# Performance work log

Hardware: AMD Instinct MI355X
Metric: run time of the kernel (lower is better)

## Reference

```python
import jax, jax.numpy as jnp
import numpy as np

N = 100000
E = 1000000
IN_FEAT = 64
OUT_FEAT = 64


def setup_inputs() -> dict:
    key = jax.random.key(0)
    k_h, k_src, k_dst, k_w, k_b = jax.random.split(key, 5)
    h = jax.random.normal(k_h, (N, IN_FEAT), dtype=jnp.float32)
    src = jax.random.randint(k_src, (E,), 0, N, dtype=jnp.int64)
    dst = jax.random.randint(k_dst, (E,), 0, N, dtype=jnp.int64)
    # nn.Linear(in_feat*2, out_feat): W is [out, 2*in], b is [out]
    bound = 1.0 / np.sqrt(2 * IN_FEAT)
    W = jax.random.uniform(k_w, (OUT_FEAT, 2 * IN_FEAT), dtype=jnp.float32, minval=-bound, maxval=bound)
    b = jax.random.uniform(k_b, (OUT_FEAT,), dtype=jnp.float32, minval=-bound, maxval=bound)
    return {"h": h, "src": src, "dst": dst, "W": W, "b": b}


def reference(h, src, dst, W, b):
    # copy_u + mean: gather src features, segment-mean over dst (in-neighbors)
    msg_sum = jax.ops.segment_sum(h[src], dst, num_segments=N)          # [N, in]
    deg = jax.ops.segment_sum(jnp.ones((src.shape[0],), h.dtype), dst, num_segments=N)  # [N]
    h_neigh = msg_sum / jnp.maximum(deg, 1.0)[:, None]                  # isolated nodes -> 0 (DGL mean)
    h_total = jnp.concatenate([h, h_neigh], axis=1)                     # [N, 2*in]
    return jax.nn.relu(h_total @ W.T + b)
```

## Files before the change

### kernel.cpp

```cpp
#include <hip/hip_runtime.h>

#define FEAT 64
#define BN 128
#define SHIFTMAXB 512
#define BCAP 4096

typedef __attribute__((ext_vector_type(8))) __bf16 bf16x8;
typedef __attribute__((ext_vector_type(8))) unsigned short ushort8;
typedef __attribute__((ext_vector_type(4))) float f32x4;

__device__ inline unsigned short f2bf(float f) {
    union { float f; unsigned u; } c; c.f = f;
    unsigned u = c.u;
    return (unsigned short)((u + 0x7fffu + ((u >> 16) & 1u)) >> 16);
}
__device__ inline float bf2f(unsigned short s) {
    union { unsigned u; float f; } c; c.u = ((unsigned)s) << 16; return c.f;
}

__global__ void __launch_bounds__(256)
zero_kernel(int* __restrict__ p)
{
    int t = threadIdx.x;
    p[t] = 0; p[t + 256] = 0;
}

__global__ void __launch_bounds__(256)
scatter_kernel(const float* __restrict__ h, unsigned short* __restrict__ hbf,
               int total8, const float* __restrict__ W,
               unsigned short* __restrict__ wfg,
               const int* __restrict__ src, const int* __restrict__ dst,
               int* __restrict__ cursors, int* __restrict__ pairs,
               int E, int shift, int h2bfB)
{
    __shared__ int hist[512];
    __shared__ int chunk[512];
    int bid = blockIdx.x, t = threadIdx.x;

    if (bid < h2bfB) {
        int i = bid * 256 + t;
        if (i < total8) {
            const float4* p = (const float4*)(h + (size_t)i * 8);
            float4 a = p[0], b = p[1];
            ushort8 v;
            v[0] = f2bf(a.x); v[1] = f2bf(a.y); v[2] = f2bf(a.z); v[3] = f2bf(a.w);
            v[4] = f2bf(b.x); v[5] = f2bf(b.y); v[6] = f2bf(b.z); v[7] = f2bf(b.w);
            *(ushort8*)(hbf + (size_t)i * 8) = v;
        }
        return;
    }
    if (bid < h2bfB + 4) {
        int i = (bid - h2bfB) * 256 + t;
        int ksnt = i >> 6, lane = i & 63;
        int row = (ksnt & 3) * 16 + (lane & 15);
        int kb  = (ksnt >> 2) * 32 + (lane >> 4) * 8;
        const float4* p = (const float4*)(W + row * 128 + kb);
        float4 a = p[0], b = p[1];
        ushort8 v;
        v[0] = f2bf(a.x); v[1] = f2bf(a.y); v[2] = f2bf(a.z); v[3] = f2bf(a.w);
        v[4] = f2bf(b.x); v[5] = f2bf(b.y); v[6] = f2bf(b.z); v[7] = f2bf(b.w);
        *(ushort8*)(wfg + i * 8) = v;
        return;
    }

    hist[t] = 0; hist[t + 256] = 0;
    __syncthreads();
    int base = (bid - h2bfB - 4) * 4096;
    int s_[16], d_[16];
    #pragma unroll
    for (int r = 0; r < 4; ++r) {
        int e = base + r * 1024 + t * 4;
        if (e + 3 < E) {
            *(int4*)&s_[r * 4] = *(const int4*)&src[e];
            *(int4*)&d_[r * 4] = *(const int4*)&dst[e];
        } else {
            #pragma unroll
            for (int j = 0; j < 4; ++j) {
                int ee = e + j;
                s_[r * 4 + j] = (ee < E) ? src[ee] : -1;
                d_[r * 4 + j] = (ee < E) ? dst[ee] : -1;
            }
        }
    }
    #pragma unroll
    for (int i = 0; i < 16; ++i)
        if (d_[i] >= 0) atomicAdd(&hist[d_[i] >> shift], 1);
    __syncthreads();
    if (hist[t])       { chunk[t]       = (t)       * BCAP + atomicAdd(&cursors[t],       hist[t]);       hist[t] = 0; }
    if (hist[t + 256]) { chunk[t + 256] = (t + 256) * BCAP + atomicAdd(&cursors[t + 256], hist[t + 256]); hist[t + 256] = 0; }
    __syncthreads();
    int mask = (1 << shift) - 1;
    #pragma unroll
    for (int i = 0; i < 16; ++i) {
        if (d_[i] >= 0) {
            int bk = d_[i] >> shift;
            int pos = atomicAdd(&hist[bk], 1);
            int at  = chunk[bk] + pos;
            if (at < (bk + 1) * BCAP)
                pairs[at] = (s_[i] << shift) | (d_[i] & mask);
        }
    }
}

__device__ inline void scan_bases(const int* __restrict__ sizes,
                                  int* __restrict__ basesl, int* __restrict__ sums)
{
    int t = threadIdx.x;
    int v0 = sizes[2 * t], v1 = sizes[2 * t + 1];
    int s = v0 + v1;
    sums[t] = s; __syncthreads();
    for (int o = 1; o < 256; o <<= 1) {
        int u = (t >= o) ? sums[t - o] : 0;
        __syncthreads();
        sums[t] += u; __syncthreads();
    }
    int ex = sums[t] - s;
    basesl[2 * t] = ex; basesl[2 * t + 1] = ex + v0;
    __syncthreads();
}

__global__ void __launch_bounds__(256)
bucket_csr_kernel(const int* __restrict__ pairs, const int* __restrict__ cursors,
                  int* __restrict__ off, int* __restrict__ adj,
                  int N, int E, int shift)
{
    __shared__ int basesl[512];
    __shared__ int sums[256];
    __shared__ int cnt[256];
    int b = blockIdx.x, t = threadIdx.x;

    scan_bases(cursors, basesl, sums);

    int nb0 = b << shift;
    int nn = min(1 << shift, N - nb0);
    int mask = (1 << shift) - 1;
    int e0 = basesl[b];
    int sz = cursors[b];
    int p0 = b * BCAP;

    cnt[t] = 0; __syncthreads();
    for (int e = t; e < sz; e += 256)
        atomicAdd(&cnt[pairs[p0 + e] & mask], 1);
    __syncthreads();
    int v = cnt[t];
    sums[t] = v; __syncthreads();
    for (int o = 1; o < 256; o <<= 1) {
        int u = (t >= o) ? sums[t - o] : 0;
        __syncthreads();
        sums[t] += u; __syncthreads();
    }
    int ex = sums[t] - v;
    if (t < nn) off[nb0 + t] = e0 + ex;
    cnt[t] = ex;
    __syncthreads();
    for (int e = t; e < sz; e += 256) {
        int pk = pairs[p0 + e];
        int pos = atomicAdd(&cnt[pk & mask], 1);
        adj[e0 + pos] = pk >> shift;
    }
    if (b == 0 && t == 0) off[N] = E;
}

__global__ void __launch_bounds__(256)
gather_kernel(const unsigned short* __restrict__ hbf, const int* __restrict__ adj,
              const int* __restrict__ off, unsigned short* __restrict__ hn,
              int N)
{
    int node = (blockIdx.x * 256 + threadIdx.x) >> 6;
    if (node >= N) return;
    int lane = threadIdx.x & 63;
    int sub = lane >> 3, f8 = lane & 7;

    int o0 = off[node], o1 = off[node + 1];
    int deg = o1 - o0;
    int adjv = (o0 + lane < o1) ? adj[o0 + lane] : 0;

    float acc[8] = {0.f, 0.f, 0.f, 0.f, 0.f, 0.f, 0.f, 0.f};
    int nb = (min(deg, 64) + 7) >> 3;
    for (int k = 0; k < nb; k += 2) {
        int eA = k * 8 + sub, eB = (k + 1) * 8 + sub;
        int iA = __shfl(adjv, eA);
        int iB = __shfl(adjv, eB);
        bool vA = eA < deg;
        bool vB = (k + 1 < nb) && (eB < deg);
        ushort8 rA, rB;
        if (vA) rA = *(const ushort8*)&hbf[(size_t)iA * FEAT + f8 * 8];
        if (vB) rB = *(const ushort8*)&hbf[(size_t)iB * FEAT + f8 * 8];
        if (vA) {
            #pragma unroll
            for (int j = 0; j < 8; ++j) acc[j] += bf2f(rA[j]);
        }
        if (vB) {
            #pragma unroll
            for (int j = 0; j < 8; ++j) acc[j] += bf2f(rB[j]);
        }
    }
    for (int base = o0 + 64; base < o1; base += 8) {
        int e = base + sub;
        if (e < o1) {
            ushort8 r = *(const ushort8*)&hbf[(size_t)adj[e] * FEAT + f8 * 8];
            #pragma unroll
            for (int j = 0; j < 8; ++j) acc[j] += bf2f(r[j]);
        }
    }
    #pragma unroll
    for (int j = 0; j < 8; ++j) {
        float v = acc[j];
        v += __shfl_xor(v, 8);
        v += __shfl_xor(v, 16);
        v += __shfl_xor(v, 32);
        acc[j] = v;
    }
    if (sub == 0) {
        float inv = 1.0f / fmaxf((float)deg, 1.0f);
        ushort8 m;
        #pragma unroll
        for (int j = 0; j < 8; ++j) m[j] = f2bf(acc[j] * inv);
        *(ushort8*)&hn[(size_t)node * 128 + f8 * 8] = m;
    }
}

__global__ void __launch_bounds__(512, 3)
sage_mfma_kernel(const unsigned short* __restrict__ hbf,
                 const unsigned short* __restrict__ hn,
                 const unsigned short* __restrict__ wfg,
                 const float* __restrict__ bias, float* __restrict__ out, int N)
{
    __shared__ unsigned short xl[BN * 128];
    __shared__ unsigned short wl[1024 * 8];

    int t = threadIdx.x;
    int lane = t & 63, w = t >> 6;
    int node0 = blockIdx.x * BN;

    #pragma unroll
    for (int it = 0; it < 2; ++it) {
        int i = t + it * 512;
        *(ushort8*)&wl[i * 8] = *(const ushort8*)&wfg[(size_t)i * 8];
    }

    #pragma unroll
    for (int it = 0; it < 2; ++it) {
        int i = t + it * 512;
        int n = i >> 3, c8 = i & 7;
        int node = node0 + n;
        ushort8 v = {};
        if (node < N) v = *(const ushort8*)&hbf[(size_t)node * FEAT + c8 * 8];
        *(ushort8*)&xl[(n * 16 + (c8 ^ (n & 7))) * 8] = v;
    }

    #pragma unroll
    for (int it = 0; it < 2; ++it) {
        int i = t + it * 512;
        int n = i >> 3, c8 = i & 7;
        int node = node0 + n;
        ushort8 v = {};
        if (node < N) v = *(const ushort8*)&hn[(size_t)node * 128 + c8 * 8];
        *(ushort8*)&xl[(n * 16 + ((8 + c8) ^ (n & 7))) * 8] = v;
    }
    __syncthreads();

    f32x4 acc[4] = {};
    int r = w * 16 + (lane & 15);
    #pragma unroll
    for (int ks = 0; ks < 4; ++ks) {
        int chunk = ks * 4 + (lane >> 4);
        bf16x8 a = *(const bf16x8*)&xl[(r * 16 + (chunk ^ (r & 7))) * 8];
        #pragma unroll
        for (int nt = 0; nt < 4; ++nt) {
            bf16x8 b = *(const bf16x8*)&wl[((ks * 4 + nt) * 64 + lane) * 8];
            acc[nt] = __builtin_amdgcn_mfma_f32_16x16x32_bf16(a, b, acc[nt], 0, 0, 0);
        }
    }

    int col   = lane & 15;
    int rbase = node0 + w * 16 + (lane >> 4) * 4;
    #pragma unroll
    for (int nt = 0; nt < 4; ++nt) {
        float bj = bias[nt * 16 + col];
        #pragma unroll
        for (int rr = 0; rr < 4; ++rr) {
            int node = rbase + rr;
            if (node < N) {
                float vv = acc[nt][rr] + bj;
                out[(size_t)node * FEAT + nt * 16 + col] = fmaxf(vv, 0.f);
            }
        }
    }
}

extern "C" void kernel_launch(void* const* d_in, const int* in_sizes, int n_in,
                              void* d_out, int out_size, void* d_ws, size_t ws_size,
                              hipStream_t stream)
{
    const float* h   = (const float*)d_in[0];
    const int*   src = (const int*)d_in[1];
    const int*   dst = (const int*)d_in[2];
    const float* W   = (const float*)d_in[3];
    const float* b   = (const float*)d_in[4];
    float* out = (float*)d_out;

    int N = in_sizes[0] / FEAT;
    int E = in_sizes[1];

    int shift = 0;
    while (((N - 1) >> shift) >= SHIFTMAXB) ++shift;
    int NB = ((N - 1) >> shift) + 1;

    unsigned short* hbf = (unsigned short*)d_ws;
    unsigned short* wfg = hbf + (size_t)N * FEAT;
    int*  pairs   = (int*)(wfg + 8192);
    int*  adj     = pairs + (size_t)512 * BCAP;
    int*  off     = adj + E;
    int*  cursors = off + (N + 1);

    zero_kernel<<<1, 256, 0, stream>>>(cursors);

    int total8 = N * (FEAT / 8);
    int h2bfB  = (total8 + 255) / 256;
    int spB    = (E + 4095) / 4096;
    scatter_kernel<<<h2bfB + 4 + spB, 256, 0, stream>>>(h, hbf, total8, W, wfg,
                                                        src, dst, cursors, pairs,
                                                        E, shift, h2bfB);

    bucket_csr_kernel<<<NB, 256, 0, stream>>>(pairs, cursors, off, adj, N, E, shift);

    unsigned short* hn = (unsigned short*)d_out;
    int gwaves = (N + 3) / 4;
    gather_kernel<<<gwaves, 256, 0, stream>>>(hbf, adj, off, hn, N);

    int gblocks = (N + BN - 1) / BN;
    sage_mfma_kernel<<<gblocks, 512, 0, stream>>>(hbf, hn, wfg, b, out, N);
}
```

Before: 89.26 us.

## Fuse neighbor gather into MFMA linear kernel via shared memory

Merges the separate gather and MFMA GEMM kernels into one kernel. Each 1024-thread block aggregates 16 nodes, one wave per node, writes the bf16 means and self features into LDS, then four waves run the 16x64 MFMA with bias and ReLU. This removes the global round trip of the intermediate neighbor buffer and one kernel launch. In exchange, every block reloads the full weight tile into LDS, and only 4 of 16 waves do the GEMM after a block-wide barrier, which may reduce gather occupancy.

```diff
diff --git a/kernel.cpp b/kernel.cpp
--- a/kernel.cpp
+++ b/kernel.cpp
@@ -1,7 +1,6 @@
 #include <hip/hip_runtime.h>
 
 #define FEAT 64
-#define BN 128
 #define SHIFTMAXB 512
 #define BCAP 4096
 
@@ -161,17 +160,31 @@
     if (b == 0 && t == 0) off[N] = E;
 }
 
-__global__ void __launch_bounds__(256)
-gather_kernel(const unsigned short* __restrict__ hbf, const int* __restrict__ adj,
-              const int* __restrict__ off, unsigned short* __restrict__ hn,
-              int N)
-{
-    int node = (blockIdx.x * 256 + threadIdx.x) >> 6;
-    if (node >= N) return;
-    int lane = threadIdx.x & 63;
+__global__ void __launch_bounds__(1024, 8)
+gather_mfma_kernel(const unsigned short* __restrict__ hbf,
+                   const int* __restrict__ adj, const int* __restrict__ off,
+                   const unsigned short* __restrict__ wfg,
+                   const float* __restrict__ bias, float* __restrict__ out, int N)
+{
+    __shared__ unsigned short xl[16 * 128];
+    __shared__ unsigned short wl[1024 * 8];
+
+    int t = threadIdx.x;
+    int lane = t & 63, w = t >> 6;
+    int node0 = blockIdx.x * 16;
+    int node = node0 + w;
+    bool valid = node < N;
     int sub = lane >> 3, f8 = lane & 7;
 
-    int o0 = off[node], o1 = off[node + 1];
+    *(ushort8*)&wl[t * 8] = *(const ushort8*)&wfg[(size_t)t * 8];
+
+    if (valid && sub == 1) {
+        ushort8 v = *(const ushort8*)&hbf[(size_t)node * FEAT + f8 * 8];
+        *(ushort8*)&xl[(w * 16 + (f8 ^ (w & 7))) * 8] = v;
+    }
+
+    int o0 = 0, o1 = 0;
+    if (valid) { o0 = off[node]; o1 = off[node + 1]; }
     int deg = o1 - o0;
     int adjv = (o0 + lane < o1) ? adj[o0 + lane] : 0;
 
@@ -211,80 +224,32 @@
         v += __shfl_xor(v, 32);
         acc[j] = v;
     }
-    if (sub == 0) {
+    if (valid && sub == 0) {
         float inv = 1.0f / fmaxf((float)deg, 1.0f);
         ushort8 m;
         #pragma unroll
         for (int j = 0; j < 8; ++j) m[j] = f2bf(acc[j] * inv);
-        *(ushort8*)&hn[(size_t)node * 128 + f8 * 8] = m;
-    }
-}
-
-__global__ void __launch_bounds__(512, 3)
-sage_mfma_kernel(const unsigned short* __restrict__ hbf,
-                 const unsigned short* __restrict__ hn,
-                 const unsigned short* __restrict__ wfg,
-                 const float* __restrict__ bias, float* __restrict__ out, int N)
-{
-    __shared__ unsigned short xl[BN * 128];
-    __shared__ unsigned short wl[1024 * 8];
-
-    int t = threadIdx.x;
-    int lane = t & 63, w = t >> 6;
-    int node0 = blockIdx.x * BN;
-
-    #pragma unroll
-    for (int it = 0; it < 2; ++it) {
-        int i = t + it * 512;
-        *(ushort8*)&wl[i * 8] = *(const ushort8*)&wfg[(size_t)i * 8];
-    }
-
-    #pragma unroll
-    for (int it = 0; it < 2; ++it) {
-        int i = t + it * 512;
-        int n = i >> 3, c8 = i & 7;
-        int node = node0 + n;
-        ushort8 v = {};
-        if (node < N) v = *(const ushort8*)&hbf[(size_t)node * FEAT + c8 * 8];
-        *(ushort8*)&xl[(n * 16 + (c8 ^ (n & 7))) * 8] = v;
-    }
-
-    #pragma unroll
-    for (int it = 0; it < 2; ++it) {
-        int i = t + it * 512;
-        int n = i >> 3, c8 = i & 7;
-        int node = node0 + n;
-        ushort8 v = {};
-        if (node < N) v = *(const ushort8*)&hn[(size_t)node * 128 + c8 * 8];
-        *(ushort8*)&xl[(n * 16 + ((8 + c8) ^ (n & 7))) * 8] = v;
-    }
-    __syncthreads();
-
-    f32x4 acc[4] = {};
-    int r = w * 16 + (lane & 15);
-    #pragma unroll
-    for (int ks = 0; ks < 4; ++ks) {
-        int chunk = ks * 4 + (lane >> 4);
-        bf16x8 a = *(const bf16x8*)&xl[(r * 16 + (chunk ^ (r & 7))) * 8];
+        *(ushort8*)&xl[(w * 16 + ((8 + f8) ^ (w & 7))) * 8] = m;
+    }
+    __syncthreads();
+
+    if (w < 4) {
+        f32x4 gacc = {};
+        int r = lane & 15;
         #pragma unroll
-        for (int nt = 0; nt < 4; ++nt) {
-            bf16x8 b = *(const bf16x8*)&wl[((ks * 4 + nt) * 64 + lane) * 8];
-            acc[nt] = __builtin_amdgcn_mfma_f32_16x16x32_bf16(a, b, acc[nt], 0, 0, 0);
-        }
-    }
-
-    int col   = lane & 15;
-    int rbase = node0 + w * 16 + (lane >> 4) * 4;
-    #pragma unroll
-    for (int nt = 0; nt < 4; ++nt) {
-        float bj = bias[nt * 16 + col];
+        for (int ks = 0; ks < 4; ++ks) {
+            int chunk = ks * 4 + (lane >> 4);
+            bf16x8 a = *(const bf16x8*)&xl[(r * 16 + (chunk ^ (r & 7))) * 8];
+            bf16x8 b = *(const bf16x8*)&wl[((ks * 4 + w) * 64 + lane) * 8];
+            gacc = __builtin_amdgcn_mfma_f32_16x16x32_bf16(a, b, gacc, 0, 0, 0);
+        }
+        int col = lane & 15;
+        float bj = bias[w * 16 + col];
         #pragma unroll
         for (int rr = 0; rr < 4; ++rr) {
-            int node = rbase + rr;
-            if (node < N) {
-                float vv = acc[nt][rr] + bj;
-                out[(size_t)node * FEAT + nt * 16 + col] = fmaxf(vv, 0.f);
-            }
+            int nd = node0 + (lane >> 4) * 4 + rr;
+            if (nd < N)
+                out[(size_t)nd * FEAT + w * 16 + col] = fmaxf(gacc[rr] + bj, 0.f);
         }
     }
 }
@@ -325,10 +290,6 @@
 
     bucket_csr_kernel<<<NB, 256, 0, stream>>>(pairs, cursors, off, adj, N, E, shift);
 
-    unsigned short* hn = (unsigned short*)d_out;
-    int gwaves = (N + 3) / 4;
-    gather_kernel<<<gwaves, 256, 0, stream>>>(hbf, adj, off, hn, N);
-
-    int gblocks = (N + BN - 1) / BN;
-    sage_mfma_kernel<<<gblocks, 512, 0, stream>>>(hbf, hn, wfg, b, out, N);
-}
+    int gblocks = (N + 15) / 16;
+    gather_mfma_kernel<<<gblocks, 1024, 0, stream>>>(hbf, adj, off, wfg, b, out, N);
+}
```

Measured after the change: 98.79 us. +10.7%, slower.

## Fuse bucket CSR build and neighbor gather into one LDS-resident kernel

Applied to the files above, without the earlier changes.

Merges the per-bucket CSR construction and the mean-aggregation gather into one kernel. Each 1024-thread block sorts its bucket's edges into a local adjacency list in shared memory, then 16 waves each aggregate 16 nodes from it. This removes the global adj/off arrays, their writes and re-reads, the cross-bucket base scan, and one kernel launch. The cost is far fewer blocks (one per bucket), with each wave walking its nodes one after another, which may hurt latency hiding and load balance across CUs.

```diff
diff --git a/kernel.cpp b/kernel.cpp
--- a/kernel.cpp
+++ b/kernel.cpp
@@ -102,121 +102,89 @@
     }
 }
 
-__device__ inline void scan_bases(const int* __restrict__ sizes,
-                                  int* __restrict__ basesl, int* __restrict__ sums)
-{
-    int t = threadIdx.x;
-    int v0 = sizes[2 * t], v1 = sizes[2 * t + 1];
-    int s = v0 + v1;
-    sums[t] = s; __syncthreads();
+__global__ void __launch_bounds__(1024, 2)
+bucket_gather_kernel(const unsigned short* __restrict__ hbf,
+                     const int* __restrict__ pairs, const int* __restrict__ cursors,
+                     unsigned short* __restrict__ hn, int N, int shift)
+{
+    __shared__ int loff[257];
+    __shared__ int cnt[256];
+    __shared__ int sums[256];
+    __shared__ int ladj[BCAP];
+    int b = blockIdx.x, t = threadIdx.x;
+    int nb0 = b << shift;
+    int sz = min(cursors[b], BCAP);
+    int p0 = b * BCAP;
+    int mask = (1 << shift) - 1;
+
+    if (t < 256) cnt[t] = 0;
+    __syncthreads();
+    for (int e = t; e < sz; e += 1024)
+        atomicAdd(&cnt[pairs[p0 + e] & mask], 1);
+    __syncthreads();
+    int v = 0;
+    if (t < 256) { v = cnt[t]; sums[t] = v; }
+    __syncthreads();
     for (int o = 1; o < 256; o <<= 1) {
-        int u = (t >= o) ? sums[t - o] : 0;
+        int u = 0;
+        if (t < 256 && t >= o) u = sums[t - o];
         __syncthreads();
-        sums[t] += u; __syncthreads();
-    }
-    int ex = sums[t] - s;
-    basesl[2 * t] = ex; basesl[2 * t + 1] = ex + v0;
-    __syncthreads();
-}
-
-__global__ void __launch_bounds__(256)
-bucket_csr_kernel(const int* __restrict__ pairs, const int* __restrict__ cursors,
-                  int* __restrict__ off, int* __restrict__ adj,
-                  int N, int E, int shift)
-{
-    __shared__ int basesl[512];
-    __shared__ int sums[256];
-    __shared__ int cnt[256];
-    int b = blockIdx.x, t = threadIdx.x;
-
-    scan_bases(cursors, basesl, sums);
-
-    int nb0 = b << shift;
-    int nn = min(1 << shift, N - nb0);
-    int mask = (1 << shift) - 1;
-    int e0 = basesl[b];
-    int sz = cursors[b];
-    int p0 = b * BCAP;
-
-    cnt[t] = 0; __syncthreads();
-    for (int e = t; e < sz; e += 256)
-        atomicAdd(&cnt[pairs[p0 + e] & mask], 1);
-    __syncthreads();
-    int v = cnt[t];
-    sums[t] = v; __syncthreads();
-    for (int o = 1; o < 256; o <<= 1) {
-        int u = (t >= o) ? sums[t - o] : 0;
+        if (t < 256) sums[t] += u;
         __syncthreads();
-        sums[t] += u; __syncthreads();
-    }
-    int ex = sums[t] - v;
-    if (t < nn) off[nb0 + t] = e0 + ex;
-    cnt[t] = ex;
-    __syncthreads();
-    for (int e = t; e < sz; e += 256) {
+    }
+    if (t < 256) {
+        loff[t] = sums[t] - v;
+        cnt[t]  = sums[t] - v;
+        if (t == 255) loff[256] = sums[255];
+    }
+    __syncthreads();
+    for (int e = t; e < sz; e += 1024) {
         int pk = pairs[p0 + e];
         int pos = atomicAdd(&cnt[pk & mask], 1);
-        adj[e0 + pos] = pk >> shift;
-    }
-    if (b == 0 && t == 0) off[N] = E;
-}
-
-__global__ void __launch_bounds__(256)
-gather_kernel(const unsigned short* __restrict__ hbf, const int* __restrict__ adj,
-              const int* __restrict__ off, unsigned short* __restrict__ hn,
-              int N)
-{
-    int node = (blockIdx.x * 256 + threadIdx.x) >> 6;
-    if (node >= N) return;
-    int lane = threadIdx.x & 63;
+        ladj[pos] = pk >> shift;
+    }
+    __syncthreads();
+
+    int lane = t & 63, w = t >> 6;
     int sub = lane >> 3, f8 = lane & 7;
-
-    int o0 = off[node], o1 = off[node + 1];
-    int deg = o1 - o0;
-    int adjv = (o0 + lane < o1) ? adj[o0 + lane] : 0;
-
-    float acc[8] = {0.f, 0.f, 0.f, 0.f, 0.f, 0.f, 0.f, 0.f};
-    int nb = (min(deg, 64) + 7) >> 3;
-    for (int k = 0; k < nb; k += 2) {
-        int eA = k * 8 + sub, eB = (k + 1) * 8 + sub;
-        int iA = __shfl(adjv, eA);
-        int iB = __shfl(adjv, eB);
-        bool vA = eA < deg;
-        bool vB = (k + 1 < nb) && (eB < deg);
-        ushort8 rA, rB;
-        if (vA) rA = *(const ushort8*)&hbf[(size_t)iA * FEAT + f8 * 8];
-        if (vB) rB = *(const ushort8*)&hbf[(size_t)iB * FEAT + f8 * 8];
-        if (vA) {
+    for (int q = 0; q < 16; ++q) {
+        int nl = w * 16 + q;
+        int node = nb0 + nl;
+        if (node >= N) break;
+        int o0 = loff[nl], o1 = loff[nl + 1];
+        int deg = o1 - o0;
+        float acc[8] = {0.f, 0.f, 0.f, 0.f, 0.f, 0.f, 0.f, 0.f};
+        for (int base = o0; base < o1; base += 16) {
+            int eA = base + sub, eB = base + 8 + sub;
+            int iA = (eA < o1) ? ladj[eA] : -1;
+            int iB = (eB < o1) ? ladj[eB] : -1;
+            ushort8 rA, rB;
+            if (iA >= 0) rA = *(const ushort8*)&hbf[(size_t)iA * FEAT + f8 * 8];
+            if (iB >= 0) rB = *(const ushort8*)&hbf[(size_t)iB * FEAT + f8 * 8];
+            if (iA >= 0) {
+                #pragma unroll
+                for (int j = 0; j < 8; ++j) acc[j] += bf2f(rA[j]);
+            }
+            if (iB >= 0) {
+                #pragma unroll
+                for (int j = 0; j < 8; ++j) acc[j] += bf2f(rB[j]);
+            }
+        }
+        #pragma unroll
+        for (int j = 0; j < 8; ++j) {
+            float x = acc[j];
+            x += __shfl_xor(x, 8);
+            x += __shfl_xor(x, 16);
+            x += __shfl_xor(x, 32);
+            acc[j] = x;
+        }
+        if (sub == 0) {
+            float inv = 1.0f / fmaxf((float)deg, 1.0f);
+            ushort8 m;
             #pragma unroll
-            for (int j = 0; j < 8; ++j) acc[j] += bf2f(rA[j]);
-        }
-        if (vB) {
-            #pragma unroll
-            for (int j = 0; j < 8; ++j) acc[j] += bf2f(rB[j]);
-        }
-    }
-    for (int base = o0 + 64; base < o1; base += 8) {
-        int e = base + sub;
-        if (e < o1) {
-            ushort8 r = *(const ushort8*)&hbf[(size_t)adj[e] * FEAT + f8 * 8];
-            #pragma unroll
-            for (int j = 0; j < 8; ++j) acc[j] += bf2f(r[j]);
-        }
-    }
-    #pragma unroll
-    for (int j = 0; j < 8; ++j) {
-        float v = acc[j];
-        v += __shfl_xor(v, 8);
-        v += __shfl_xor(v, 16);
-        v += __shfl_xor(v, 32);
-        acc[j] = v;
-    }
-    if (sub == 0) {
-        float inv = 1.0f / fmaxf((float)deg, 1.0f);
-        ushort8 m;
-        #pragma unroll
-        for (int j = 0; j < 8; ++j) m[j] = f2bf(acc[j] * inv);
-        *(ushort8*)&hn[(size_t)node * 128 + f8 * 8] = m;
+            for (int j = 0; j < 8; ++j) m[j] = f2bf(acc[j] * inv);
+            *(ushort8*)&hn[(size_t)node * 128 + f8 * 8] = m;
+        }
     }
 }
 
@@ -310,9 +278,7 @@
     unsigned short* hbf = (unsigned short*)d_ws;
     unsigned short* wfg = hbf + (size_t)N * FEAT;
     int*  pairs   = (int*)(wfg + 8192);
-    int*  adj     = pairs + (size_t)512 * BCAP;
-    int*  off     = adj + E;
-    int*  cursors = off + (N + 1);
+    int*  cursors = pairs + (size_t)512 * BCAP;
 
     zero_kernel<<<1, 256, 0, stream>>>(cursors);
 
@@ -323,11 +289,8 @@
                                                         src, dst, cursors, pairs,
                                                         E, shift, h2bfB);
 
-    bucket_csr_kernel<<<NB, 256, 0, stream>>>(pairs, cursors, off, adj, N, E, shift);
-
     unsigned short* hn = (unsigned short*)d_out;
-    int gwaves = (N + 3) / 4;
-    gather_kernel<<<gwaves, 256, 0, stream>>>(hbf, adj, off, hn, N);
+    bucket_gather_kernel<<<NB, 1024, 0, stream>>>(hbf, pairs, cursors, hn, N, shift);
 
     int gblocks = (N + BN - 1) / BN;
     sage_mfma_kernel<<<gblocks, 512, 0, stream>>>(hbf, hn, wfg, b, out, N);
```

Result: no change. 90.29 us (+1.2%).
